# Kernel optimization log

Hardware: AMD Instinct MI355X
Metric: run time of the kernel (lower is better)

The kernel has to match this reference:

```python
import jax, jax.numpy as jnp
import numpy as np

NGRAPH = 200   # batched graphs
NPG = 100      # nodes per graph
N = NGRAPH * NPG
EPG = 800      # edges per graph
E = NGRAPH * EPG
IN_DIM = 21
HID = 256      # nodes (hidden width)
NHEAD = 1
NLAYER = 4
EPS = 1e-5
SLOPE = 0.2    # GATv2 leaky_relu negative slope


def _edge_softmax(score, dst):
    # score: [E, H]; softmax over incoming edges of each dst node
    m = jax.ops.segment_max(score, dst, num_segments=N)
    m = jnp.where(jnp.isfinite(m), m, 0.0)
    ex = jnp.exp(score - m[dst])
    den = jax.ops.segment_sum(ex, dst, num_segments=N)
    return ex / den[dst]


def _gat(h, src, dst, Ws, bs, Wd, bd, a, res):
    # GATv2Conv: share_weights=False, residual, allow_zero_in_degree
    Hh, Dd = a.shape
    fs = (h @ Ws + bs).reshape(N, Hh, Dd)
    fd = (h @ Wd + bd).reshape(N, Hh, Dd)
    e = jax.nn.leaky_relu(fs[src] + fd[dst], SLOPE)          # [E,H,D]
    score = jnp.einsum('ehd,hd->eh', e, a)                    # [E,H]
    alpha = _edge_softmax(score, dst)                         # [E,H]
    rst = jax.ops.segment_sum(alpha[:, :, None] * fs[src], dst, num_segments=N)
    return (rst + res.reshape(N, Hh, Dd)).reshape(N, Hh * Dd), alpha


def _bn(x, g, b):
    # BatchNorm1d, training-mode batch stats (biased var), affine
    mu = x.mean(0)
    var = x.var(0)
    return g * (x - mu) / jnp.sqrt(var + EPS) + b


def _graph_mean(h, gid):
    s = jax.ops.segment_sum(h, gid, num_segments=NGRAPH)
    cnt = jax.ops.segment_sum(jnp.ones((h.shape[0], 1), h.dtype), gid, num_segments=NGRAPH)
    return s / cnt


def _forward(x, Ws0, bs0, Wd0, bd0, a0, Wres0, g0, be0,
             Ws_r, bs_r, Wd_r, bd_r, a_r, g_r, be_r,
             fc1_W, fc1_b, gfc, bfc, fc2_W, fc2_b, src, dst, gid):
    feats, attns = [], []
    h, al = _gat(x, src, dst, Ws0, bs0, Wd0, bd0, a0, x @ Wres0)
    h = jax.nn.relu(_bn(h, g0, be0))
    feats.append(_graph_mean(h, gid)); attns.append(al[:, 0])
    for l in range(NLAYER - 1):
        h2, al = _gat(h, src, dst, Ws_r[l], bs_r[l], Wd_r[l], bd_r[l], a_r[l], h)
        h = jax.nn.relu(_bn(h2, g_r[l], be_r[l]))
        feats.append(_graph_mean(h, gid)); attns.append(al[:, 0])
    feat = jnp.concatenate(feats, axis=1)                     # [B, NLAYER*HID]
    feat = jax.nn.relu(_bn(feat @ fc1_W + fc1_b, gfc, bfc))   # dropout is identity (eval)
    feat = feat @ fc2_W + fc2_b                               # [B, 5]
    attns = jnp.stack(attns).T                                # [E, NLAYER]
    return feat, attns


def setup_inputs() -> dict:
    key = jax.random.key(0)
    ks = jax.random.split(key, 24)
    sc = 0.05
    eoff = jnp.repeat(jnp.arange(NGRAPH, dtype=jnp.int32) * NPG, EPG)
    src = jax.random.randint(ks[0], (E,), 0, NPG, dtype=jnp.int32) + eoff
    dst = jax.random.randint(ks[1], (E,), 0, NPG, dtype=jnp.int32) + eoff
    gid = jnp.repeat(jnp.arange(NGRAPH, dtype=jnp.int32), NPG)
    return {
        'x': jax.random.normal(ks[2], (N, IN_DIM), jnp.float32),
        'Ws0': jax.random.normal(ks[3], (IN_DIM, HID), jnp.float32) * sc,
        'bs0': jnp.zeros((HID,), jnp.float32),
        'Wd0': jax.random.normal(ks[4], (IN_DIM, HID), jnp.float32) * sc,
        'bd0': jnp.zeros((HID,), jnp.float32),
        'a0': jax.random.normal(ks[5], (NHEAD, HID // NHEAD), jnp.float32) * sc,
        'Wres0': jax.random.normal(ks[6], (IN_DIM, HID), jnp.float32) * sc,
        'g0': jnp.ones((HID,), jnp.float32),
        'be0': jnp.zeros((HID,), jnp.float32),
        'Ws_r': jax.random.normal(ks[7], (NLAYER - 1, HID, HID), jnp.float32) * sc,
        'bs_r': jnp.zeros((NLAYER - 1, HID), jnp.float32),
        'Wd_r': jax.random.normal(ks[8], (NLAYER - 1, HID, HID), jnp.float32) * sc,
        'bd_r': jnp.zeros((NLAYER - 1, HID), jnp.float32),
        'a_r': jax.random.normal(ks[9], (NLAYER - 1, NHEAD, HID // NHEAD), jnp.float32) * sc,
        'g_r': jnp.ones((NLAYER - 1, HID), jnp.float32),
        'be_r': jnp.zeros((NLAYER - 1, HID), jnp.float32),
        'fc1_W': jax.random.normal(ks[10], (NLAYER * HID, HID), jnp.float32) * sc,
        'fc1_b': jnp.zeros((HID,), jnp.float32),
        'gfc': jnp.ones((HID,), jnp.float32),
        'bfc': jnp.zeros((HID,), jnp.float32),
        'fc2_W': jax.random.normal(ks[11], (HID, 5), jnp.float32) * sc,
        'fc2_b': jnp.zeros((5,), jnp.float32),
        'src': src, 'dst': dst, 'gid': gid,
    }


def reference(x, Ws0, bs0, Wd0, bd0, a0, Wres0, g0, be0,
              Ws_r, bs_r, Wd_r, bd_r, a_r, g_r, be_r,
              fc1_W, fc1_b, gfc, bfc, fc2_W, fc2_b, src, dst, gid):
    return _forward(x, Ws0, bs0, Wd0, bd0, a0, Wres0, g0, be0,
                    Ws_r, bs_r, Wd_r, bd_r, a_r, g_r, be_r,
                    fc1_W, fc1_b, gfc, bfc, fc2_W, fc2_b, src, dst, gid)
```

## Files before the change

### kernel.cpp

```cpp
#include <hip/hip_runtime.h>

typedef __bf16 bf16x8 __attribute__((ext_vector_type(8)));
typedef __bf16 bf16x4 __attribute__((ext_vector_type(4)));
typedef float f32x4 __attribute__((ext_vector_type(4)));

constexpr int cN   = 20000;
constexpr int cG   = 200;
constexpr int cNPG = 100;
constexpr int cE   = 160000;
constexpr int cEPG = 800;
constexpr int cHID = 256;
constexpr int cIN  = 21;
constexpr float cEPS   = 1e-5f;
constexpr float cSLOPE = 0.2f;
constexpr int cCH  = 32;
constexpr int cCHS = 25;

__device__ __forceinline__ float4 cvt4(bf16x4 v) {
    return make_float4((float)v.x, (float)v.y, (float)v.z, (float)v.w);
}

__device__ __forceinline__ void gl_lds16(const __bf16* g, __bf16* l) {
    __builtin_amdgcn_global_load_lds(
        (const __attribute__((address_space(1))) void*)g,
        (__attribute__((address_space(3))) void*)l, 16, 0, 0);
}

__global__ __launch_bounds__(256) void k_in_gemm(
    const float* __restrict__ x,
    const float* __restrict__ Ws, const float* __restrict__ bs,
    const float* __restrict__ Wd, const float* __restrict__ bd,
    const float* __restrict__ Wr,
    __bf16* __restrict__ fsb, __bf16* __restrict__ fdb, __bf16* __restrict__ resb)
{
    __shared__ float xl[8 * cIN];
    int tid = threadIdx.x;
    int rb  = blockIdx.x * 8;
    if (tid < 8 * cIN) xl[tid] = x[(size_t)rb * cIN + tid];
    __syncthreads();
    int j = tid;
    float ws[cIN], wd[cIN], wr[cIN];
#pragma unroll
    for (int k = 0; k < cIN; ++k) {
        ws[k] = Ws[k * cHID + j];
        wd[k] = Wd[k * cHID + j];
        wr[k] = Wr[k * cHID + j];
    }
    float vbs = bs[j], vbd = bd[j];
    for (int r = 0; r < 8; ++r) {
        float as = vbs, ad = vbd, ar = 0.f;
#pragma unroll
        for (int k = 0; k < cIN; ++k) {
            float xv = xl[r * cIN + k];
            as += xv * ws[k];
            ad += xv * wd[k];
            ar += xv * wr[k];
        }
        size_t o = (size_t)(rb + r) * cHID + j;
        fsb[o] = (__bf16)as; fdb[o] = (__bf16)ad; resb[o] = (__bf16)ar;
    }
}

__global__ __launch_bounds__(256) void k_wcvt(
    const float* __restrict__ Ws_r, const float* __restrict__ Wd_r,
    __bf16* __restrict__ WT)
{
    int mat = blockIdx.y;
    int l = mat >> 1;
    const float* W = ((mat & 1) ? Wd_r : Ws_r) + (size_t)l * cHID * cHID;
    __bf16* T = WT + (size_t)l * 512 * cHID + (size_t)(mat & 1) * cHID * cHID;
    int k = blockIdx.x, n = threadIdx.x;
    T[(size_t)n * cHID + k] = (__bf16)W[(size_t)k * cHID + n];
}

__global__ __launch_bounds__(256) void k_gemm_mfma(
    const __bf16* __restrict__ hb, const __bf16* __restrict__ Wcat,
    const float* __restrict__ bs, const float* __restrict__ bd,
    __bf16* __restrict__ fsb, __bf16* __restrict__ fdb)
{
    __shared__ __bf16 lA[128 * 32];
    __shared__ __bf16 lB[128 * 32];
    int tid = threadIdx.x, lane = tid & 63, w = tid >> 6;
    int wr = w >> 1, wc = w & 1;
    int rc = lane & 15, kg = lane >> 4;
    int m0  = blockIdx.x * 128;
    int bn0 = blockIdx.y * 128;

    f32x4 acc[4][4];
#pragma unroll
    for (int m = 0; m < 4; ++m)
#pragma unroll
        for (int n = 0; n < 4; ++n)
            acc[m][n] = (f32x4){0.f, 0.f, 0.f, 0.f};

#pragma unroll 1
    for (int ks = 0; ks < 8; ++ks) {
        int k0 = ks * 32;
#pragma unroll
        for (int j = 0; j < 2; ++j) {
            int c   = j * 256 + tid;
            int row = c >> 2, ci = c & 3;
            __bf16* dA = &lA[(size_t)(j * 256 + w * 64) * 8];
            __bf16* dB = &lB[(size_t)(j * 256 + w * 64) * 8];
            gl_lds16(hb   + (size_t)(m0  + row) * cHID + k0 + ci * 8, dA);
            gl_lds16(Wcat + (size_t)(bn0 + row) * cHID + k0 + ci * 8, dB);
        }
        __syncthreads();

        bf16x8 a[4], b[4];
#pragma unroll
        for (int m = 0; m < 4; ++m)
            a[m] = *(const bf16x8*)&lA[(wr * 64 + m * 16 + rc) * 32 + kg * 8];
#pragma unroll
        for (int n = 0; n < 4; ++n)
            b[n] = *(const bf16x8*)&lB[(wc * 64 + n * 16 + rc) * 32 + kg * 8];
#pragma unroll
        for (int m = 0; m < 4; ++m)
#pragma unroll
            for (int n = 0; n < 4; ++n)
                acc[m][n] = __builtin_amdgcn_mfma_f32_16x16x32_bf16(a[m], b[n], acc[m][n], 0, 0, 0);
        __syncthreads();
    }

#pragma unroll
    for (int m = 0; m < 4; ++m) {
        int rbase = m0 + wr * 64 + m * 16 + kg * 4;
#pragma unroll
        for (int n = 0; n < 4; ++n) {
            int col = bn0 + wc * 64 + n * 16 + rc;
            bool isS = col < cHID;
            int  cc  = isS ? col : col - cHID;
            float bias = isS ? bs[cc] : bd[cc];
            __bf16* dst = isS ? fsb : fdb;
#pragma unroll
            for (int i = 0; i < 4; ++i) {
                int r = rbase + i;
                if (r < cN)
                    dst[(size_t)r * cHID + cc] = (__bf16)(acc[m][n][i] + bias);
            }
        }
    }
}

__global__ __launch_bounds__(256) void k_csr(
    const int* __restrict__ dst, int* __restrict__ csr,
    int* __restrict__ off, int* __restrict__ deg)
{
    __shared__ int dstl[cEPG];
    __shared__ int cnt[cCH * 128];
    __shared__ int offl[cNPG];
    __shared__ int tot[128];
    int g = blockIdx.x, tid = threadIdx.x;
    int nb = g * cNPG, eb = g * cEPG;

    for (int i = tid; i < cEPG; i += 256) dstl[i] = dst[eb + i] - nb;
    for (int i = tid; i < cCH * 128; i += 256) cnt[i] = 0;
    __syncthreads();

    for (int i = tid; i < cEPG; i += 256)
        atomicAdd(&cnt[(i / cCHS) * 128 + dstl[i]], 1);
    __syncthreads();

    int mytot = 0;
    if (tid < cNPG) {
        int run = 0;
        for (int c = 0; c < cCH; ++c) {
            int t = cnt[c * 128 + tid];
            cnt[c * 128 + tid] = run;
            run += t;
        }
        mytot = run;
    }
    if (tid < 128) tot[tid] = (tid < cNPG) ? mytot : 0;
    __syncthreads();
    for (int ofs = 1; ofs < 128; ofs <<= 1) {
        int t = 0;
        if (tid < 128 && tid >= ofs) t = tot[tid - ofs];
        __syncthreads();
        if (tid < 128) tot[tid] += t;
        __syncthreads();
    }
    if (tid < cNPG) {
        int excl = tot[tid] - mytot;
        offl[tid] = excl;
        off[nb + tid] = eb + excl;
        deg[nb + tid] = mytot;
    }
    __syncthreads();

    if (tid < cCH) {
        for (int j = 0; j < cCHS; ++j) {
            int i = tid * cCHS + j;
            int n = dstl[i];
            int k = cnt[tid * 128 + n]++;
            csr[eb + offl[n] + k] = eb + i;
        }
    }
}

__global__ __launch_bounds__(256) void k_edge2(
    const __bf16* __restrict__ fsb, const __bf16* __restrict__ fdb,
    const __bf16* __restrict__ resb, const float* __restrict__ avec,
    const int* __restrict__ csr, const int* __restrict__ off,
    const int* __restrict__ deg, const int* __restrict__ src,
    float* __restrict__ hpre, float* __restrict__ attn_out,
    float* __restrict__ spill, float* __restrict__ bnz)
{
    __shared__ int   sidx[4][64];
    __shared__ int   eidx[4][64];
    __shared__ float exbuf[4][64];
    int tid = threadIdx.x, lane = tid & 63, w = tid >> 6;
    if (blockIdx.x == 0) {
        bnz[tid] = 0.f;
        bnz[tid + 256] = 0.f;
    }
    int bid = blockIdx.x;
    int g   = bid % cG;
    int nid = g * cNPG + (bid / cG) * 4 + w;
    int dg = deg[nid], base = off[nid];

    for (int i = lane; i < dg && i < 64; i += 64) {
        int e = csr[base + i];
        eidx[w][i] = e;
        sidx[w][i] = src[e];
    }

    float4 a4  = *(const float4*)(avec + lane * 4);
    float4 fd4 = cvt4(*(const bf16x4*)(fdb + (size_t)nid * cHID + lane * 4));
    float4 r4  = cvt4(*(const bf16x4*)(resb + (size_t)nid * cHID + lane * 4));

    float den = 0.f;
    float4 acc = {0.f, 0.f, 0.f, 0.f};
    for (int i = 0; i < dg; ++i) {
        int s = (i < 64) ? sidx[w][i] : src[csr[base + i]];
        float4 f4 = cvt4(*(const bf16x4*)(fsb + (size_t)s * cHID + lane * 4));
        float v0 = f4.x + fd4.x, v1 = f4.y + fd4.y;
        float v2 = f4.z + fd4.z, v3 = f4.w + fd4.w;
        v0 = v0 > 0.f ? v0 : cSLOPE * v0;
        v1 = v1 > 0.f ? v1 : cSLOPE * v1;
        v2 = v2 > 0.f ? v2 : cSLOPE * v2;
        v3 = v3 > 0.f ? v3 : cSLOPE * v3;
        float part = v0 * a4.x + v1 * a4.y + v2 * a4.z + v3 * a4.w;
#pragma unroll
        for (int o = 32; o; o >>= 1) part += __shfl_xor(part, o);
        float ex = __expf(part);
        den += ex;
        acc.x += ex * f4.x; acc.y += ex * f4.y;
        acc.z += ex * f4.z; acc.w += ex * f4.w;
        if (lane == 0) {
            if (i < 64) exbuf[w][i] = ex;
            else        spill[csr[base + i]] = ex;
        }
    }
    float inv = (dg > 0) ? 1.f / den : 0.f;

    for (int i = lane; i < dg; i += 64) {
        float ex = (i < 64) ? exbuf[w][i] : spill[csr[base + i]];
        int e    = (i < 64) ? eidx[w][i]  : csr[base + i];
        attn_out[(size_t)e * 4] = ex * inv;
    }

    float4 o4 = {acc.x * inv + r4.x, acc.y * inv + r4.y,
                 acc.z * inv + r4.z, acc.w * inv + r4.w};
    *(float4*)(hpre + (size_t)nid * cHID + lane * 4) = o4;
}

__global__ __launch_bounds__(256) void k_bn_stats(
    const float* __restrict__ hpre, float* __restrict__ gsum, float* __restrict__ gssq,
    float* __restrict__ featcat_l)
{
    int j = threadIdx.x, g = blockIdx.x, q = blockIdx.y;
    if (q == 0) featcat_l[(size_t)g * (4 * cHID) + j] = 0.f;
    int rb = g * cNPG + q * 50;
    float s = 0.f, qq = 0.f;
    for (int r = 0; r < 50; ++r) {
        float v = hpre[(size_t)(rb + r) * cHID + j];
        s += v; qq += v * v;
    }
    atomicAdd(&gsum[j], s);
    atomicAdd(&gssq[j], qq);
}

__global__ __launch_bounds__(256) void k_bn_apply(
    const float* __restrict__ hpre,
    const float* __restrict__ gsum, const float* __restrict__ gssq,
    const float* __restrict__ gamma, const float* __restrict__ beta,
    __bf16* __restrict__ hb, float* __restrict__ featcat_l)
{
    int j = threadIdx.x, g = blockIdx.x, q = blockIdx.y;
    float mu  = gsum[j] * (1.f / cN);
    float var = gssq[j] * (1.f / cN) - mu * mu;
    float sc  = gamma[j] * rsqrtf(var + cEPS);
    float sh  = beta[j] - mu * sc;
    float fsum = 0.f;
    int r0 = g * cNPG + q * 25;
    for (int r = 0; r < 25; ++r) {
        size_t i = (size_t)(r0 + r) * cHID + j;
        float v = hpre[i] * sc + sh;
        v = v > 0.f ? v : 0.f;
        hb[i] = (__bf16)v;
        fsum += v;
    }
    atomicAdd(&featcat_l[(size_t)g * (4 * cHID) + j], fsum * (1.f / cNPG));
}

__global__ __launch_bounds__(256) void k_fc1(
    const float* __restrict__ featcat, const float* __restrict__ W,
    const float* __restrict__ b, float* __restrict__ out)
{
    __shared__ float row[4 * cHID];
    int g = blockIdx.x, j = threadIdx.x;
    for (int i = j; i < 4 * cHID; i += 256) row[i] = featcat[(size_t)g * (4 * cHID) + i];
    __syncthreads();
    float acc = b[j];
    for (int k = 0; k < 4 * cHID; ++k) acc += row[k] * W[(size_t)k * cHID + j];
    out[(size_t)g * cHID + j] = acc;
}

__global__ __launch_bounds__(256) void k_fc_bn(
    float* __restrict__ f2, const float* __restrict__ gamma, const float* __restrict__ beta)
{
    int j = threadIdx.x;
    float s = 0.f, q = 0.f;
    for (int r = 0; r < cG; ++r) { float v = f2[(size_t)r * cHID + j]; s += v; q += v * v; }
    float mu  = s * (1.f / cG);
    float var = q * (1.f / cG) - mu * mu;
    float sc  = gamma[j] * rsqrtf(var + cEPS);
    float sh  = beta[j] - mu * sc;
    for (int r = 0; r < cG; ++r) {
        float v = f2[(size_t)r * cHID + j] * sc + sh;
        f2[(size_t)r * cHID + j] = v > 0.f ? v : 0.f;
    }
}

__global__ __launch_bounds__(256) void k_fc2(
    const float* __restrict__ f2, const float* __restrict__ W,
    const float* __restrict__ b, float* __restrict__ out)
{
    int t = blockIdx.x * 256 + threadIdx.x;
    if (t >= cG * 5) return;
    int r = t / 5, o = t % 5;
    float acc = b[o];
    for (int k = 0; k < cHID; ++k) acc += f2[(size_t)r * cHID + k] * W[k * 5 + o];
    out[t] = acc;
}

extern "C" void kernel_launch(void* const* d_in, const int* in_sizes, int n_in,
                              void* d_out, int out_size, void* d_ws, size_t ws_size,
                              hipStream_t stream)
{
    (void)in_sizes; (void)n_in; (void)out_size; (void)ws_size;
    const float* x     = (const float*)d_in[0];
    const float* Ws0   = (const float*)d_in[1];
    const float* bs0   = (const float*)d_in[2];
    const float* Wd0   = (const float*)d_in[3];
    const float* bd0   = (const float*)d_in[4];
    const float* a0    = (const float*)d_in[5];
    const float* Wres0 = (const float*)d_in[6];
    const float* g0    = (const float*)d_in[7];
    const float* be0   = (const float*)d_in[8];
    const float* Ws_r  = (const float*)d_in[9];
    const float* bs_r  = (const float*)d_in[10];
    const float* Wd_r  = (const float*)d_in[11];
    const float* bd_r  = (const float*)d_in[12];
    const float* a_r   = (const float*)d_in[13];
    const float* g_r   = (const float*)d_in[14];
    const float* be_r  = (const float*)d_in[15];
    const float* fc1_W = (const float*)d_in[16];
    const float* fc1_b = (const float*)d_in[17];
    const float* gfc   = (const float*)d_in[18];
    const float* bfc   = (const float*)d_in[19];
    const float* fc2_W = (const float*)d_in[20];
    const float* fc2_b = (const float*)d_in[21];
    const int*   src   = (const int*)d_in[22];
    const int*   dst   = (const int*)d_in[23];
    float* out = (float*)d_out;

    char* p = (char*)d_ws;
    float* hpre    = (float*)p; p += (size_t)cN * cHID * 4;
    float* featcat = (float*)p; p += (size_t)cG * 4 * cHID * 4;
    float* feat2   = (float*)p; p += (size_t)cG * cHID * 4;
    float* gsum    = (float*)p; p += cHID * 4;
    float* gssq    = (float*)p; p += cHID * 4;
    float* spill   = (float*)p; p += (size_t)cE * 4;
    int*   csr     = (int*)p;   p += (size_t)cE * 4;
    int*   offv    = (int*)p;   p += (size_t)cN * 4;
    int*   degv    = (int*)p;   p += (size_t)cN * 4;
    __bf16* hb     = (__bf16*)p; p += (size_t)cN * cHID * 2;
    __bf16* resb0  = (__bf16*)p; p += (size_t)cN * cHID * 2;
    __bf16* fsb    = (__bf16*)p; p += (size_t)cN * cHID * 2;
    __bf16* fdb    = (__bf16*)p; p += (size_t)cN * cHID * 2;
    __bf16* WT     = (__bf16*)p; p += (size_t)3 * 512 * cHID * 2;

    k_wcvt<<<dim3(cHID, 6), 256, 0, stream>>>(Ws_r, Wd_r, WT);
    k_csr<<<cG, 256, 0, stream>>>(dst, csr, offv, degv);

    k_in_gemm<<<cN / 8, 256, 0, stream>>>(x, Ws0, bs0, Wd0, bd0, Wres0, fsb, fdb, resb0);

    for (int l = 0; l < 4; ++l) {
        if (l > 0) {
            k_gemm_mfma<<<dim3(157, 4), 256, 0, stream>>>(
                hb,
                WT + (size_t)(l - 1) * 512 * cHID,
                bs_r + (size_t)(l - 1) * cHID, bd_r + (size_t)(l - 1) * cHID,
                fsb, fdb);
        }
        const float* ap = (l == 0) ? a0 : a_r + (size_t)(l - 1) * cHID;
        const __bf16* rb = (l == 0) ? resb0 : hb;
        k_edge2<<<cN / 4, 256, 0, stream>>>(fsb, fdb, rb, ap, csr, offv, degv, src,
                                            hpre, out + 1000 + l, spill, gsum);
        float* fcl = featcat + (size_t)l * cHID;
        k_bn_stats<<<dim3(cG, 2), 256, 0, stream>>>(hpre, gsum, gssq, fcl);
        const float* gm = (l == 0) ? g0  : g_r  + (size_t)(l - 1) * cHID;
        const float* bt = (l == 0) ? be0 : be_r + (size_t)(l - 1) * cHID;
        k_bn_apply<<<dim3(cG, 4), 256, 0, stream>>>(hpre, gsum, gssq, gm, bt, hb, fcl);
    }

    k_fc1<<<cG, 256, 0, stream>>>(featcat, fc1_W, fc1_b, feat2);
    k_fc_bn<<<1, 256, 0, stream>>>(feat2, gfc, bfc);
    k_fc2<<<4, 256, 0, stream>>>(feat2, fc2_W, fc2_b, out);
}
```

Before: 333.3 us.

## Process four edges per wavefront iteration in GAT aggregation kernel

The per-node attention kernel now splits each 64-lane wavefront into four 16-lane groups, each handling a different incoming edge. Each lane covers 16 feature dims instead of 4. This cuts the serial loop trip count by four and shortens the score reduction from six shuffles to four. In exchange it adds cross-group reductions of the accumulators at the end, uses more registers, and leaves lanes idle when the degree is not a multiple of four.

```diff
diff --git a/kernel.cpp b/kernel.cpp
--- a/kernel.cpp
+++ b/kernel.cpp
@@ -218,6 +218,7 @@
     int g   = bid % cG;
     int nid = g * cNPG + (bid / cG) * 4 + w;
     int dg = deg[nid], base = off[nid];
+    int grp = lane >> 4, l16 = lane & 15;
 
     for (int i = lane; i < dg && i < 64; i += 64) {
         int e = csr[base + i];
@@ -225,33 +226,63 @@
         sidx[w][i] = src[e];
     }
 
-    float4 a4  = *(const float4*)(avec + lane * 4);
-    float4 fd4 = cvt4(*(const bf16x4*)(fdb + (size_t)nid * cHID + lane * 4));
-    float4 r4  = cvt4(*(const bf16x4*)(resb + (size_t)nid * cHID + lane * 4));
+    float4 a4[4], fd4[4];
+#pragma unroll
+    for (int j = 0; j < 4; ++j) {
+        int d = l16 * 4 + j * 64;
+        a4[j]  = *(const float4*)(avec + d);
+        fd4[j] = cvt4(*(const bf16x4*)(fdb + (size_t)nid * cHID + d));
+    }
 
     float den = 0.f;
-    float4 acc = {0.f, 0.f, 0.f, 0.f};
-    for (int i = 0; i < dg; ++i) {
-        int s = (i < 64) ? sidx[w][i] : src[csr[base + i]];
-        float4 f4 = cvt4(*(const bf16x4*)(fsb + (size_t)s * cHID + lane * 4));
-        float v0 = f4.x + fd4.x, v1 = f4.y + fd4.y;
-        float v2 = f4.z + fd4.z, v3 = f4.w + fd4.w;
-        v0 = v0 > 0.f ? v0 : cSLOPE * v0;
-        v1 = v1 > 0.f ? v1 : cSLOPE * v1;
-        v2 = v2 > 0.f ? v2 : cSLOPE * v2;
-        v3 = v3 > 0.f ? v3 : cSLOPE * v3;
-        float part = v0 * a4.x + v1 * a4.y + v2 * a4.z + v3 * a4.w;
-#pragma unroll
-        for (int o = 32; o; o >>= 1) part += __shfl_xor(part, o);
-        float ex = __expf(part);
+    f32x4 acc[4];
+#pragma unroll
+    for (int j = 0; j < 4; ++j) acc[j] = (f32x4){0.f, 0.f, 0.f, 0.f};
+
+    for (int it = 0; it * 4 < dg; ++it) {
+        int i = it * 4 + grp;
+        bool on = i < dg;
+        int s = on ? ((i < 64) ? sidx[w][i] : src[csr[base + i]]) : 0;
+        const __bf16* fsp = fsb + (size_t)s * cHID + l16 * 4;
+        float4 f4[4];
+        float part = 0.f;
+#pragma unroll
+        for (int j = 0; j < 4; ++j) {
+            f4[j] = cvt4(*(const bf16x4*)(fsp + j * 64));
+            float v0 = f4[j].x + fd4[j].x, v1 = f4[j].y + fd4[j].y;
+            float v2 = f4[j].z + fd4[j].z, v3 = f4[j].w + fd4[j].w;
+            v0 = v0 > 0.f ? v0 : cSLOPE * v0;
+            v1 = v1 > 0.f ? v1 : cSLOPE * v1;
+            v2 = v2 > 0.f ? v2 : cSLOPE * v2;
+            v3 = v3 > 0.f ? v3 : cSLOPE * v3;
+            part += v0 * a4[j].x + v1 * a4[j].y + v2 * a4[j].z + v3 * a4[j].w;
+        }
+        part += __shfl_xor(part, 1);
+        part += __shfl_xor(part, 2);
+        part += __shfl_xor(part, 4);
+        part += __shfl_xor(part, 8);
+        float ex = on ? __expf(part) : 0.f;
         den += ex;
-        acc.x += ex * f4.x; acc.y += ex * f4.y;
-        acc.z += ex * f4.z; acc.w += ex * f4.w;
-        if (lane == 0) {
+#pragma unroll
+        for (int j = 0; j < 4; ++j) {
+            acc[j][0] += ex * f4[j].x; acc[j][1] += ex * f4[j].y;
+            acc[j][2] += ex * f4[j].z; acc[j][3] += ex * f4[j].w;
+        }
+        if (on && l16 == 0) {
             if (i < 64) exbuf[w][i] = ex;
             else        spill[csr[base + i]] = ex;
         }
     }
+
+    den += __shfl_xor(den, 16);
+    den += __shfl_xor(den, 32);
+#pragma unroll
+    for (int j = 0; j < 4; ++j)
+#pragma unroll
+        for (int k = 0; k < 4; ++k) {
+            acc[j][k] += __shfl_xor(acc[j][k], 16);
+            acc[j][k] += __shfl_xor(acc[j][k], 32);
+        }
     float inv = (dg > 0) ? 1.f / den : 0.f;
 
     for (int i = lane; i < dg; i += 64) {
@@ -260,9 +291,11 @@
         attn_out[(size_t)e * 4] = ex * inv;
     }
 
-    float4 o4 = {acc.x * inv + r4.x, acc.y * inv + r4.y,
-                 acc.z * inv + r4.z, acc.w * inv + r4.w};
-    *(float4*)(hpre + (size_t)nid * cHID + lane * 4) = o4;
+    int dw = l16 * 4 + grp * 64;
+    float4 r4 = cvt4(*(const bf16x4*)(resb + (size_t)nid * cHID + dw));
+    float4 o4 = {acc[grp][0] * inv + r4.x, acc[grp][1] * inv + r4.y,
+                 acc[grp][2] * inv + r4.z, acc[grp][3] * inv + r4.w};
+    *(float4*)(hpre + (size_t)nid * cHID + dw) = o4;
 }
 
 __global__ __launch_bounds__(256) void k_bn_stats(
```

Measured after the change: 340.3 us. 2.1% more time.

## Fuse BatchNorm statistics accumulation into the edge aggregation kernel

Applied to the files above, without the earlier changes.

Removes the separate BN-stats kernel: each edge block stages its four output rows in shared memory and atomically adds per-column sums and sums of squares. Zeroing of the stat buffers moves into the preceding GEMM kernels, and featcat zeroing moves into the edge kernel. This saves a launch and a full re-read of hpre per layer, at the cost of many more global atomics (one pair per column per block) contending on the same 512 addresses.

```diff
diff --git a/kernel.cpp b/kernel.cpp
--- a/kernel.cpp
+++ b/kernel.cpp
@@ -31,10 +31,12 @@
     const float* __restrict__ Ws, const float* __restrict__ bs,
     const float* __restrict__ Wd, const float* __restrict__ bd,
     const float* __restrict__ Wr,
-    __bf16* __restrict__ fsb, __bf16* __restrict__ fdb, __bf16* __restrict__ resb)
+    __bf16* __restrict__ fsb, __bf16* __restrict__ fdb, __bf16* __restrict__ resb,
+    float* __restrict__ bnz)
 {
     __shared__ float xl[8 * cIN];
     int tid = threadIdx.x;
+    if (blockIdx.x == 0) { bnz[tid] = 0.f; bnz[tid + 256] = 0.f; }
     int rb  = blockIdx.x * 8;
     if (tid < 8 * cIN) xl[tid] = x[(size_t)rb * cIN + tid];
     __syncthreads();
@@ -76,11 +78,13 @@
 __global__ __launch_bounds__(256) void k_gemm_mfma(
     const __bf16* __restrict__ hb, const __bf16* __restrict__ Wcat,
     const float* __restrict__ bs, const float* __restrict__ bd,
-    __bf16* __restrict__ fsb, __bf16* __restrict__ fdb)
+    __bf16* __restrict__ fsb, __bf16* __restrict__ fdb,
+    float* __restrict__ bnz)
 {
     __shared__ __bf16 lA[128 * 32];
     __shared__ __bf16 lB[128 * 32];
     int tid = threadIdx.x, lane = tid & 63, w = tid >> 6;
+    if (blockIdx.x == 0 && blockIdx.y == 0) { bnz[tid] = 0.f; bnz[tid + 256] = 0.f; }
     int wr = w >> 1, wc = w & 1;
     int rc = lane & 15, kg = lane >> 4;
     int m0  = blockIdx.x * 128;
@@ -204,17 +208,17 @@
     const int* __restrict__ csr, const int* __restrict__ off,
     const int* __restrict__ deg, const int* __restrict__ src,
     float* __restrict__ hpre, float* __restrict__ attn_out,
-    float* __restrict__ spill, float* __restrict__ bnz)
+    float* __restrict__ spill, float* __restrict__ gsum,
+    float* __restrict__ gssq, float* __restrict__ fcl)
 {
     __shared__ int   sidx[4][64];
     __shared__ int   eidx[4][64];
     __shared__ float exbuf[4][64];
+    __shared__ float hblk[4][256];
     int tid = threadIdx.x, lane = tid & 63, w = tid >> 6;
-    if (blockIdx.x == 0) {
-        bnz[tid] = 0.f;
-        bnz[tid + 256] = 0.f;
-    }
     int bid = blockIdx.x;
+    if (bid < cG)
+        fcl[(size_t)bid * (4 * cHID) + tid] = 0.f;
     int g   = bid % cG;
     int nid = g * cNPG + (bid / cG) * 4 + w;
     int dg = deg[nid], base = off[nid];
@@ -263,22 +267,12 @@
     float4 o4 = {acc.x * inv + r4.x, acc.y * inv + r4.y,
                  acc.z * inv + r4.z, acc.w * inv + r4.w};
     *(float4*)(hpre + (size_t)nid * cHID + lane * 4) = o4;
-}
-
-__global__ __launch_bounds__(256) void k_bn_stats(
-    const float* __restrict__ hpre, float* __restrict__ gsum, float* __restrict__ gssq,
-    float* __restrict__ featcat_l)
-{
-    int j = threadIdx.x, g = blockIdx.x, q = blockIdx.y;
-    if (q == 0) featcat_l[(size_t)g * (4 * cHID) + j] = 0.f;
-    int rb = g * cNPG + q * 50;
-    float s = 0.f, qq = 0.f;
-    for (int r = 0; r < 50; ++r) {
-        float v = hpre[(size_t)(rb + r) * cHID + j];
-        s += v; qq += v * v;
-    }
-    atomicAdd(&gsum[j], s);
-    atomicAdd(&gssq[j], qq);
+    *(float4*)&hblk[w][lane * 4] = o4;
+    __syncthreads();
+
+    float v0 = hblk[0][tid], v1 = hblk[1][tid], v2 = hblk[2][tid], v3 = hblk[3][tid];
+    atomicAdd(&gsum[tid], v0 + v1 + v2 + v3);
+    atomicAdd(&gssq[tid], v0 * v0 + v1 * v1 + v2 * v2 + v3 * v3);
 }
 
 __global__ __launch_bounds__(256) void k_bn_apply(
@@ -395,7 +389,8 @@
     k_wcvt<<<dim3(cHID, 6), 256, 0, stream>>>(Ws_r, Wd_r, WT);
     k_csr<<<cG, 256, 0, stream>>>(dst, csr, offv, degv);
 
-    k_in_gemm<<<cN / 8, 256, 0, stream>>>(x, Ws0, bs0, Wd0, bd0, Wres0, fsb, fdb, resb0);
+    k_in_gemm<<<cN / 8, 256, 0, stream>>>(x, Ws0, bs0, Wd0, bd0, Wres0,
+                                          fsb, fdb, resb0, gsum);
 
     for (int l = 0; l < 4; ++l) {
         if (l > 0) {
@@ -403,14 +398,14 @@
                 hb,
                 WT + (size_t)(l - 1) * 512 * cHID,
                 bs_r + (size_t)(l - 1) * cHID, bd_r + (size_t)(l - 1) * cHID,
-                fsb, fdb);
+                fsb, fdb, gsum);
         }
         const float* ap = (l == 0) ? a0 : a_r + (size_t)(l - 1) * cHID;
         const __bf16* rb = (l == 0) ? resb0 : hb;
+        float* fcl = featcat + (size_t)l * cHID;
         k_edge2<<<cN / 4, 256, 0, stream>>>(fsb, fdb, rb, ap, csr, offv, degv, src,
-                                            hpre, out + 1000 + l, spill, gsum);
-        float* fcl = featcat + (size_t)l * cHID;
-        k_bn_stats<<<dim3(cG, 2), 256, 0, stream>>>(hpre, gsum, gssq, fcl);
+                                            hpre, out + 1000 + l, spill,
+                                            gsum, gssq, fcl);
         const float* gm = (l == 0) ? g0  : g_r  + (size_t)(l - 1) * cHID;
         const float* bt = (l == 0) ? be0 : be_r + (size_t)(l - 1) * cHID;
         k_bn_apply<<<dim3(cG, 4), 256, 0, stream>>>(hpre, gsum, gssq, gm, bt, hb, fcl);
```

Result: slower. 701.7 us (+110.6%).
